# Kernel tuning notes

Hardware: AMD Instinct MI355X
Metric: run time of the kernel (lower is better)

Reference implementation:

```python
import jax, jax.numpy as jnp
import numpy as np

B, H, W, C, NH = 4, 64, 64, 512, 16
HD = C // NH
BIAS_LEVEL = 0.1
LN_EPS = 1e-5


def layernorm(x, g, b):
    m = jnp.mean(x, axis=-1, keepdims=True)
    v = jnp.mean(jnp.square(x - m), axis=-1, keepdims=True)
    return (x - m) * jax.lax.rsqrt(v + LN_EPS) * g + b


def partition(x, idx):
    # x: [B, L, C] -> windows [nW, S, C]
    xg = x.reshape(B, H, W, C)
    if idx == 0:  # horizontal strips: window = one row of length W
        return xg.reshape(B * H, W, C)
    else:  # vertical strips: window = one column of length H, ordered by column
        return xg.transpose(0, 2, 1, 3).reshape(B * W, H, C)


def unpartition(w, idx):
    # w: [nW, S, C] -> [B, L, C]
    if idx == 0:
        return w.reshape(B, H * W, C)
    else:
        return w.reshape(B, W, H, C).transpose(0, 2, 1, 3).reshape(B, H * W, C)


def eg_attention(q, k, v, res_x, rpe, idx):
    # q,k,v: [B, L, C]; res_x: [B, L, C]; rpe: [1, NH, S, S]
    S = rpe.shape[-1]
    nW = (B * H * W) // S

    def to_heads(t):
        return partition(t, idx).reshape(nW, S, NH, HD).transpose(0, 2, 1, 3)

    qh, kh, vh = to_heads(q), to_heads(k), to_heads(v)  # [nW, NH, S, HD]
    attn = jnp.einsum('whsd,whtd->whst', qh, kh) + BIAS_LEVEL * rpe
    # gating mask from raw scores
    M = jnp.mean(jnp.abs(attn), axis=(1, 2, 3), keepdims=True)  # [nW,1,1,1]
    M = M / jnp.max(M)
    M = jnp.maximum(M, 0.5)
    # L2-normalize rows, trig transform
    norm = jnp.sqrt(jnp.sum(jnp.square(attn), axis=-1, keepdims=True))
    attn = attn / jnp.maximum(norm, 1e-12)
    attn = 1.0 - jnp.cos(attn * (jnp.pi / 2))
    attn = attn * M
    out = jnp.einsum('whst,whtd->whsd', attn, vh)  # [nW, NH, S, HD]
    out = out.transpose(0, 2, 1, 3).reshape(nW, S, C)
    out = unpartition(out, idx)  # [B, L, C]
    # masked residual: res_x is chunked sequentially (row-major), as in the source
    res = res_x.reshape(nW, S, C) * (1.0 - M[:, 0])
    res = res.reshape(B, H * W, C)
    return out + res


def eg_block(x, rpe, idx, ln1_g, ln1_b, wqkv, wproj, bproj, ln2_g, ln2_b,
             wfc1, bfc1, wfc2, bfc2):
    img = layernorm(x, ln1_g, ln1_b)
    qkv = img @ wqkv  # [B, L, 3C]
    q, k, v = jnp.split(qkv, 3, axis=-1)
    att = eg_attention(q, k, v, x, rpe, idx)
    att = att @ wproj + bproj
    x = x + att
    h = layernorm(x, ln2_g, ln2_b)
    h = jax.nn.gelu(h @ wfc1 + bfc1, approximate=False) @ wfc2 + bfc2
    return x + h


def setup_inputs() -> dict:
    key = jax.random.key(0)
    ks = jax.random.split(key, 16)
    d = {
        'x': jax.random.normal(ks[0], (B, H * W, C), jnp.float32),
        'rpe0': jax.random.normal(ks[1], (1, NH, W, W), jnp.float32),
        'rpe1': jax.random.normal(ks[2], (1, NH, H, H), jnp.float32),
    }
    for i, blk in enumerate(['0', '1']):
        kk = jax.random.split(ks[3 + i], 8)
        d['ln1_g' + blk] = jnp.ones((C,), jnp.float32)
        d['ln1_b' + blk] = jnp.zeros((C,), jnp.float32)
        d['wqkv' + blk] = jax.random.normal(kk[0], (C, 3 * C), jnp.float32) * 0.02
        d['wproj' + blk] = jax.random.normal(kk[1], (C, C), jnp.float32) * 0.02
        d['bproj' + blk] = jnp.zeros((C,), jnp.float32)
        d['ln2_g' + blk] = jnp.ones((C,), jnp.float32)
        d['ln2_b' + blk] = jnp.zeros((C,), jnp.float32)
        d['wfc1_' + blk] = jax.random.normal(kk[2], (C, 4 * C), jnp.float32) * 0.02
        d['bfc1_' + blk] = jnp.zeros((4 * C,), jnp.float32)
        d['wfc2_' + blk] = jax.random.normal(kk[3], (4 * C, C), jnp.float32) * 0.02
        d['bfc2_' + blk] = jnp.zeros((C,), jnp.float32)
    return d


def reference(x, rpe0, rpe1,
              ln1_g0, ln1_b0, wqkv0, wproj0, bproj0, ln2_g0, ln2_b0,
              wfc1_0, bfc1_0, wfc2_0, bfc2_0,
              ln1_g1, ln1_b1, wqkv1, wproj1, bproj1, ln2_g1, ln2_b1,
              wfc1_1, bfc1_1, wfc2_1, bfc2_1):
    x = eg_block(x, rpe0, 0, ln1_g0, ln1_b0, wqkv0, wproj0, bproj0,
                 ln2_g0, ln2_b0, wfc1_0, bfc1_0, wfc2_0, bfc2_0)
    x = eg_block(x, rpe1, 1, ln1_g1, ln1_b1, wqkv1, wproj1, bproj1,
                 ln2_g1, ln2_b1, wfc1_1, bfc1_1, wfc2_1, bfc2_1)
    return x
```

## Files before the change

kernel.cpp:

```cpp
#include <hip/hip_runtime.h>
#include <cstdint>
#include <cstddef>

typedef __bf16 bf16;
typedef __attribute__((ext_vector_type(4))) float f32x4;
typedef __attribute__((ext_vector_type(8))) __bf16 bf16x8;
typedef __attribute__((ext_vector_type(4))) __bf16 bf16x4;

static __device__ __forceinline__ f32x4 mfma16(bf16x8 a, bf16x8 b, f32x4 c) {
    return __builtin_amdgcn_mfma_f32_16x16x32_bf16(a, b, c, 0, 0, 0);
}

#define GLOAD_LDS16(gsrc, ldst)                                              \
    __builtin_amdgcn_global_load_lds(                                        \
        (const __attribute__((address_space(1))) void*)(gsrc),               \
        (__attribute__((address_space(3))) void*)(ldst), 16, 0, 0)

struct TransArgs {
    const float* W[8];
    bf16* Wt[8];
    int K[8];
    int N[8];
    int blk0[9];
};

__global__ __launch_bounds__(256)
void transpose_all(TransArgs a) {
    __shared__ float tile[32][33];
    const int b = blockIdx.x;
    int j = 0;
    #pragma unroll
    for (int i = 0; i < 7; ++i)
        if (b >= a.blk0[i + 1]) j = i + 1;
    const int rel = b - a.blk0[j];
    const int K = a.K[j], N = a.N[j];
    const int nxb = N >> 5;
    const int n0 = (rel % nxb) * 32, k0 = (rel / nxb) * 32;
    const float* W = a.W[j];
    bf16* Wt = a.Wt[j];
    const int tx = threadIdx.x & 31, ty = threadIdx.x >> 5;
    #pragma unroll
    for (int i = ty; i < 32; i += 8)
        tile[i][tx] = W[(size_t)(k0 + i) * N + n0 + tx];
    __syncthreads();
    #pragma unroll
    for (int i = ty; i < 32; i += 8)
        Wt[(size_t)(n0 + i) * K + k0 + tx] = (bf16)tile[tx][i];
}

__global__ __launch_bounds__(256)
void ln_kernel(const float* __restrict__ x, const float* __restrict__ g,
               const float* __restrict__ b, bf16* __restrict__ out) {
    const int row = blockIdx.x * 4 + (threadIdx.x >> 6);
    const int lane = threadIdx.x & 63;
    const float* p = x + (size_t)row * 512 + lane * 8;
    const float4 a0 = *(const float4*)p;
    const float4 a1 = *(const float4*)(p + 4);
    float vx[8] = {a0.x, a0.y, a0.z, a0.w, a1.x, a1.y, a1.z, a1.w};
    float s = 0.f, ss = 0.f;
    #pragma unroll
    for (int k = 0; k < 8; ++k) { s += vx[k]; ss += vx[k] * vx[k]; }
    #pragma unroll
    for (int m = 1; m < 64; m <<= 1) {
        s  += __shfl_xor(s, m);
        ss += __shfl_xor(ss, m);
    }
    const float mean = s * (1.0f / 512.0f);
    const float var  = ss * (1.0f / 512.0f) - mean * mean;
    const float inv  = rsqrtf(var + 1e-5f);
    const int c0 = lane * 8;
    const float4 g0 = *(const float4*)&g[c0], g1 = *(const float4*)&g[c0 + 4];
    const float4 b0 = *(const float4*)&b[c0], b1 = *(const float4*)&b[c0 + 4];
    const float gv[8] = {g0.x, g0.y, g0.z, g0.w, g1.x, g1.y, g1.z, g1.w};
    const float bv[8] = {b0.x, b0.y, b0.z, b0.w, b1.x, b1.y, b1.z, b1.w};
    bf16x8 o;
    #pragma unroll
    for (int k = 0; k < 8; ++k)
        o[k] = (bf16)((vx[k] - mean) * inv * gv[k] + bv[k]);
    *(bf16x8*)&out[(size_t)row * 512 + c0] = o;
}

template <int EPI, int KT>
__global__ __launch_bounds__(512, 8)
void gemm_bt(const bf16* __restrict__ A, const bf16* __restrict__ Bt,
             int N, int Krt, const float* __restrict__ bias,
             const float* __restrict__ res, float* __restrict__ outf,
             bf16* __restrict__ outh) {
    const int K = (KT > 0) ? KT : Krt;
    __shared__ __align__(16) bf16 smem[16384];
    auto lsA = [&](int buf) { return smem + buf * 4096; };
    auto lsB = [&](int buf) { return smem + 8192 + buf * 4096; };
    const int nx = gridDim.x;
    const int nwg = nx * gridDim.y;
    const int flat = blockIdx.y * nx + blockIdx.x;
    const int cpx = nwg >> 3;
    const int bswz = (flat & 7) * cpx + (flat >> 3);
    const int bn = bswz % nx, bm = bswz / nx;

    const int tid = threadIdx.x, lane = tid & 63, wv = tid >> 6;
    const int wr = wv >> 2, wc = wv & 3;
    const int l15 = lane & 15, lg = lane >> 4;
    const size_t abase = (size_t)bm * 128 * K;
    const size_t bbase = (size_t)bn * 128 * K;
    const int sr = wv * 16 + (lane >> 2);
    const int ks = ((lane & 3) ^ ((sr >> 1) & 3)) * 8;
    const bf16* aSrc = &A[abase + (size_t)sr * K + ks];
    const bf16* bSrc = &Bt[bbase + (size_t)sr * K + ks];

    f32x4 acc[4][2] = {};

    auto stage = [&](int buf, int kt) {
        GLOAD_LDS16(aSrc + kt, lsA(buf) + wv * 512);
        GLOAD_LDS16(bSrc + kt, lsB(buf) + wv * 512);
    };
    auto compute = [&](int buf) {
        bf16x8 af[4], bfr[2];
        #pragma unroll
        for (int i = 0; i < 4; ++i) {
            const int r = wr * 64 + i * 16 + l15;
            af[i] = *(const bf16x8*)
                (lsA(buf) + r * 32 + ((lg ^ ((r >> 1) & 3)) * 8));
        }
        #pragma unroll
        for (int j = 0; j < 2; ++j) {
            const int r = wc * 32 + j * 16 + l15;
            bfr[j] = *(const bf16x8*)
                (lsB(buf) + r * 32 + ((lg ^ ((r >> 1) & 3)) * 8));
        }
        #pragma unroll
        for (int i = 0; i < 4; ++i)
            #pragma unroll
            for (int j = 0; j < 2; ++j)
                acc[i][j] = mfma16(af[i], bfr[j], acc[i][j]);
    };

    if constexpr (KT > 0) {
        constexpr int NK = KT >> 5;
        stage(0, 0);
        __syncthreads();
        #pragma unroll
        for (int t = 0; t < NK - 1; ++t) {
            stage((t + 1) & 1, (t + 1) * 32);
            compute(t & 1);
            __syncthreads();
        }
        compute((NK - 1) & 1);
        __syncthreads();
    } else {
        const int NK = K >> 5;
        stage(0, 0);
        __syncthreads();
        int cur = 0;
        for (int t = 0; t < NK - 1; ++t) {
            stage(cur ^ 1, (t + 1) * 32);
            compute(cur);
            __syncthreads();
            cur ^= 1;
        }
        compute(cur);
        __syncthreads();
    }

    float* lsW = (float*)smem + wv * 1024;
    const int orow = bm * 128 + wr * 64;
    const int ocol = bn * 128 + wc * 32;
    #pragma unroll
    for (int i = 0; i < 4; ++i) {
        #pragma unroll
        for (int r = 0; r < 4; ++r)
            #pragma unroll
            for (int j = 0; j < 2; ++j)
                lsW[(lg * 4 + r) * 36 + j * 16 + l15] = acc[i][j][r];
        __builtin_amdgcn_s_waitcnt(0);
        if constexpr (EPI == 0 || EPI == 2) {
            const int rl = lane >> 2, c8 = (lane & 3) * 8;
            const float4 v0 = *(const float4*)&lsW[rl * 36 + c8];
            const float4 v1 = *(const float4*)&lsW[rl * 36 + c8 + 4];
            float vv[8] = {v0.x, v0.y, v0.z, v0.w, v1.x, v1.y, v1.z, v1.w};
            if constexpr (EPI == 2) {
                const float4 bb0 = *(const float4*)&bias[ocol + c8];
                const float4 bb1 = *(const float4*)&bias[ocol + c8 + 4];
                const float bv[8] = {bb0.x, bb0.y, bb0.z, bb0.w,
                                     bb1.x, bb1.y, bb1.z, bb1.w};
                #pragma unroll
                for (int e = 0; e < 8; ++e) {
                    const float t = vv[e] + bv[e];
                    vv[e] = 0.5f * t * (1.0f + erff(t * 0.70710678118f));
                }
            }
            bf16x8 o;
            #pragma unroll
            for (int e = 0; e < 8; ++e) o[e] = (bf16)vv[e];
            *(bf16x8*)&outh[(size_t)(orow + i * 16 + rl) * N + ocol + c8] = o;
        } else {
            const int c4 = (lane & 7) * 4;
            const float4 bb = *(const float4*)&bias[ocol + c4];
            #pragma unroll
            for (int ii = 0; ii < 2; ++ii) {
                const int rl = ii * 8 + (lane >> 3);
                const size_t gro = (size_t)(orow + i * 16 + rl) * N + ocol + c4;
                float4 v = *(const float4*)&lsW[rl * 36 + c4];
                const float4 rr = *(const float4*)&res[gro];
                v.x += bb.x + rr.x; v.y += bb.y + rr.y;
                v.z += bb.z + rr.z; v.w += bb.w + rr.w;
                *(float4*)&outf[gro] = v;
            }
        }
    }
}

__global__ __launch_bounds__(256)
void attn_stats(const bf16* __restrict__ qkv, const float* __restrict__ rpe,
                float* __restrict__ Mraw4, int idx) {
    __shared__ float lsum[4];
    const int bid = blockIdx.x;
    const int w = bid >> 2;
    const int tid = threadIdx.x, lane = tid & 63, wv = tid >> 6;
    const int h = (bid & 3) * 4 + wv;
    const int l15 = lane & 15, lg = lane >> 4;
    const long gbase = (idx == 0) ? (long)w * 64 : ((long)(w >> 6) * 4096 + (w & 63));
    const long gstride = (idx == 0) ? 1 : 64;
    bf16x8 kf[4];
    #pragma unroll
    for (int i = 0; i < 4; ++i) {
        const long gs = gbase + (long)(i * 16 + l15) * gstride;
        kf[i] = *(const bf16x8*)&qkv[gs * 1536 + 512 + h * 32 + lg * 8];
    }
    const float* rh = rpe + h * 4096;
    float asum = 0.f;
    #pragma unroll
    for (int mi = 0; mi < 4; ++mi) {
        const long gs = gbase + (long)(mi * 16 + l15) * gstride;
        const bf16x8 qf = *(const bf16x8*)&qkv[gs * 1536 + h * 32 + lg * 8];
        f32x4 sc[4] = {};
        #pragma unroll
        for (int ni = 0; ni < 4; ++ni) sc[ni] = mfma16(qf, kf[ni], sc[ni]);
        #pragma unroll
        for (int r = 0; r < 4; ++r) {
            const int srow = mi * 16 + lg * 4 + r;
            #pragma unroll
            for (int ni = 0; ni < 4; ++ni)
                asum += fabsf(sc[ni][r] + 0.1f * rh[srow * 64 + ni * 16 + l15]);
        }
    }
    #pragma unroll
    for (int m = 1; m < 64; m <<= 1) asum += __shfl_xor(asum, m);
    if (lane == 0) lsum[wv] = asum;
    __syncthreads();
    if (tid == 0) Mraw4[bid] = lsum[0] + lsum[1] + lsum[2] + lsum[3];
}

__global__ __launch_bounds__(256)
void mcalc(const float* __restrict__ Mraw4, float* __restrict__ Mv) {
    __shared__ float red[4];
    const int t = threadIdx.x, lane = t & 63;
    const float v = (Mraw4[t * 4] + Mraw4[t * 4 + 1] + Mraw4[t * 4 + 2] +
                     Mraw4[t * 4 + 3]) * (1.0f / 65536.0f);
    float m = v;
    #pragma unroll
    for (int msk = 1; msk < 64; msk <<= 1) m = fmaxf(m, __shfl_xor(m, msk));
    if (lane == 0) red[t >> 6] = m;
    __syncthreads();
    const float mm = fmaxf(fmaxf(red[0], red[1]), fmaxf(red[2], red[3]));
    Mv[t] = fmaxf(v / mm, 0.5f);
}

__global__ __launch_bounds__(256)
void attn_apply(const bf16* __restrict__ qkv, const float* __restrict__ rpe,
                const float* __restrict__ Mv, const float* __restrict__ xin,
                bf16* __restrict__ attout, int idx) {
    __shared__ __align__(16) bf16 lsP[4][64 * 64];
    __shared__ __align__(16) bf16 lsVt[4][32 * 64];
    const int bid = blockIdx.x;
    const int w = bid >> 2;
    const int tid = threadIdx.x, lane = tid & 63, wv = tid >> 6;
    const int h = (bid & 3) * 4 + wv;
    const int l15 = lane & 15, lg = lane >> 4;
    const long gbase = (idx == 0) ? (long)w * 64 : ((long)(w >> 6) * 4096 + (w & 63));
    const long gstride = (idx == 0) ? 1 : 64;
    const float Mw = Mv[w];
    bf16* P  = lsP[wv];
    bf16* Vt = lsVt[wv];

    {
        const int d4 = (lane & 7) * 4;
        #pragma unroll
        for (int it = 0; it < 8; ++it) {
            const int t = it * 8 + (lane >> 3);
            const bf16x4 v = *(const bf16x4*)
                &qkv[(gbase + (long)t * gstride) * 1536 + 1024 + h * 32 + d4];
            #pragma unroll
            for (int e = 0; e < 4; ++e) {
                const int d = d4 + e;
                Vt[d * 64 + (t ^ ((d & 7) * 8))] = v[e];
            }
        }
    }
    bf16x8 kf[4];
    #pragma unroll
    for (int i = 0; i < 4; ++i) {
        const long gs = gbase + (long)(i * 16 + l15) * gstride;
        kf[i] = *(const bf16x8*)&qkv[gs * 1536 + 512 + h * 32 + lg * 8];
    }
    const float* rh = rpe + h * 4096;
    #pragma unroll
    for (int mi = 0; mi < 4; ++mi) {
        const long gs = gbase + (long)(mi * 16 + l15) * gstride;
        const bf16x8 qf = *(const bf16x8*)&qkv[gs * 1536 + h * 32 + lg * 8];
        f32x4 sc[4] = {};
        #pragma unroll
        for (int ni = 0; ni < 4; ++ni) sc[ni] = mfma16(qf, kf[ni], sc[ni]);
        #pragma unroll
        for (int r = 0; r < 4; ++r) {
            const int srow = mi * 16 + lg * 4 + r;
            float vv[4], ssq = 0.f;
            #pragma unroll
            for (int ni = 0; ni < 4; ++ni) {
                const float v = sc[ni][r] + 0.1f * rh[srow * 64 + ni * 16 + l15];
                vv[ni] = v;
                ssq += v * v;
            }
            ssq += __shfl_xor(ssq, 1);
            ssq += __shfl_xor(ssq, 2);
            ssq += __shfl_xor(ssq, 4);
            ssq += __shfl_xor(ssq, 8);
            const float is = 1.0f / fmaxf(sqrtf(ssq), 1e-12f);
            #pragma unroll
            for (int ni = 0; ni < 4; ++ni) {
                const float v = (1.0f - __cosf(vv[ni] * is * 1.57079632679f)) * Mw;
                const int col = ni * 16 + l15;
                P[srow * 64 + (col ^ ((srow & 7) * 8))] = (bf16)v;
            }
        }
    }
    f32x4 acc[4][2] = {};
    #pragma unroll
    for (int kk = 0; kk < 2; ++kk) {
        bf16x8 bfr[2];
        #pragma unroll
        for (int dj = 0; dj < 2; ++dj) {
            const int d = dj * 16 + l15;
            bfr[dj] = *(const bf16x8*)&Vt[d * 64 + ((kk * 32 + lg * 8) ^ ((d & 7) * 8))];
        }
        #pragma unroll
        for (int mi = 0; mi < 4; ++mi) {
            const int s = mi * 16 + l15;
            const bf16x8 af = *(const bf16x8*)&P[s * 64 + ((kk * 32 + lg * 8) ^ ((s & 7) * 8))];
            #pragma unroll
            for (int dj = 0; dj < 2; ++dj)
                acc[mi][dj] = mfma16(af, bfr[dj], acc[mi][dj]);
        }
    }
    #pragma unroll
    for (int mi = 0; mi < 4; ++mi) {
        #pragma unroll
        for (int r = 0; r < 4; ++r) {
            const int s = mi * 16 + lg * 4 + r;
            const long gg = gbase + (long)s * gstride;
            const float rm = 1.0f - Mv[(int)(gg >> 6)];
            #pragma unroll
            for (int dj = 0; dj < 2; ++dj) {
                const int d = dj * 16 + l15;
                const size_t oidx = (size_t)gg * 512 + h * 32 + d;
                attout[oidx] = (bf16)(acc[mi][dj][r] + xin[oidx] * rm);
            }
        }
    }
}

extern "C" void kernel_launch(void* const* d_in, const int* in_sizes, int n_in,
                              void* d_out, int out_size, void* d_ws, size_t ws_size,
                              hipStream_t stream) {
    const float* x    = (const float*)d_in[0];
    const float* rpe0 = (const float*)d_in[1];
    const float* rpe1 = (const float*)d_in[2];
    auto W = [&](int i) { return (const float*)d_in[i]; };

    char* ws = (char*)d_ws;
    size_t off = 0;
    auto alloc = [&](size_t bytes) {
        void* p = ws + off;
        off += (bytes + 255) & ~(size_t)255;
        return p;
    };
    bf16 *wqkvT[2], *wprojT[2], *wfc1T[2], *wfc2T[2];
    for (int b = 0; b < 2; ++b) {
        wqkvT[b] = (bf16*)alloc((size_t)1536 * 512 * 2);
        wprojT[b] = (bf16*)alloc((size_t)512 * 512 * 2);
        wfc1T[b] = (bf16*)alloc((size_t)2048 * 512 * 2);
        wfc2T[b] = (bf16*)alloc((size_t)512 * 2048 * 2);
    }
    bf16* IMG = (bf16*)alloc((size_t)16384 * 512 * 2);
    bf16* QKV = (bf16*)alloc((size_t)16384 * 1536 * 2);
    bf16* ATT = (bf16*)alloc((size_t)16384 * 512 * 2);
    bf16* H1  = QKV;
    float* X1    = (float*)alloc((size_t)16384 * 512 * 4);
    float* Mraw4 = (float*)alloc(1024 * 4);
    float* Mv    = (float*)alloc(256 * 4);
    float* XMID  = (float*)d_out;

    TransArgs ta;
    const int widx[8] = {5, 6, 10, 12, 16, 17, 21, 23};
    bf16* wdst[8] = {wqkvT[0], wprojT[0], wfc1T[0], wfc2T[0],
                     wqkvT[1], wprojT[1], wfc1T[1], wfc2T[1]};
    const int wk[8] = {512, 512, 512, 2048, 512, 512, 512, 2048};
    const int wn[8] = {1536, 512, 2048, 512, 1536, 512, 2048, 512};
    int acc_b = 0;
    for (int i = 0; i < 8; ++i) {
        ta.W[i] = W(widx[i]);
        ta.Wt[i] = wdst[i];
        ta.K[i] = wk[i];
        ta.N[i] = wn[i];
        ta.blk0[i] = acc_b;
        acc_b += (wn[i] / 32) * (wk[i] / 32);
    }
    ta.blk0[8] = acc_b;
    transpose_all<<<acc_b, 256, 0, stream>>>(ta);

    for (int b = 0; b < 2; ++b) {
        const float* xin = (b == 0) ? x : X1;
        const float* rpe = (b == 0) ? rpe0 : rpe1;
        const int base = (b == 0) ? 3 : 14;
        const float* ln1g = W(base + 0);
        const float* ln1b = W(base + 1);
        const float* bproj = W(base + 4);
        const float* ln2g = W(base + 5);
        const float* ln2b = W(base + 6);
        const float* bfc1 = W(base + 8);
        const float* bfc2 = W(base + 10);

        ln_kernel<<<4096, 256, 0, stream>>>(xin, ln1g, ln1b, IMG);
        gemm_bt<0, 512><<<dim3(12, 128), 512, 0, stream>>>(
            IMG, wqkvT[b], 1536, 512, nullptr, nullptr, nullptr, QKV);
        attn_stats<<<1024, 256, 0, stream>>>(QKV, rpe, Mraw4, b);
        mcalc<<<1, 256, 0, stream>>>(Mraw4, Mv);
        attn_apply<<<1024, 256, 0, stream>>>(QKV, rpe, Mv, xin, ATT, b);
        gemm_bt<1, 512><<<dim3(4, 128), 512, 0, stream>>>(
            ATT, wprojT[b], 512, 512, bproj, xin, XMID, nullptr);
        ln_kernel<<<4096, 256, 0, stream>>>(XMID, ln2g, ln2b, IMG);
        gemm_bt<2, 512><<<dim3(16, 128), 512, 0, stream>>>(
            IMG, wfc1T[b], 2048, 512, bfc1, nullptr, nullptr, H1);
        gemm_bt<1, 0><<<dim3(4, 128), 512, 0, stream>>>(
            H1, wfc2T[b], 512, 2048, bfc2, XMID, (b == 0) ? X1 : XMID, nullptr);
    }
    (void)in_sizes; (void)n_in; (void)out_size; (void)ws_size;
}
```

Baseline: 436.1 us.

## Store intermediate residual streams in bf16 and fold mask calc into attn_apply

New measurement: 460.2 us. 5.5% more time.

```diff
diff --git a/kernel.cpp b/kernel.cpp
--- a/kernel.cpp
+++ b/kernel.cpp
@@ -15,6 +15,20 @@
     __builtin_amdgcn_global_load_lds(                                        \
         (const __attribute__((address_space(1))) void*)(gsrc),               \
         (__attribute__((address_space(3))) void*)(ldst), 16, 0, 0)
+
+template <typename T>
+static __device__ __forceinline__ void load8(const T* p, float* v) {
+    if constexpr (sizeof(T) == 4) {
+        const float4 a0 = *(const float4*)p;
+        const float4 a1 = *(const float4*)(p + 4);
+        v[0] = a0.x; v[1] = a0.y; v[2] = a0.z; v[3] = a0.w;
+        v[4] = a1.x; v[5] = a1.y; v[6] = a1.z; v[7] = a1.w;
+    } else {
+        const bf16x8 a = *(const bf16x8*)p;
+        #pragma unroll
+        for (int e = 0; e < 8; ++e) v[e] = (float)a[e];
+    }
+}
 
 struct TransArgs {
     const float* W[8];
@@ -48,15 +62,14 @@
         Wt[(size_t)(n0 + i) * K + k0 + tx] = (bf16)tile[tx][i];
 }
 
+template <typename T>
 __global__ __launch_bounds__(256)
-void ln_kernel(const float* __restrict__ x, const float* __restrict__ g,
+void ln_kernel(const T* __restrict__ x, const float* __restrict__ g,
                const float* __restrict__ b, bf16* __restrict__ out) {
     const int row = blockIdx.x * 4 + (threadIdx.x >> 6);
     const int lane = threadIdx.x & 63;
-    const float* p = x + (size_t)row * 512 + lane * 8;
-    const float4 a0 = *(const float4*)p;
-    const float4 a1 = *(const float4*)(p + 4);
-    float vx[8] = {a0.x, a0.y, a0.z, a0.w, a1.x, a1.y, a1.z, a1.w};
+    float vx[8];
+    load8(x + (size_t)row * 512 + lane * 8, vx);
     float s = 0.f, ss = 0.f;
     #pragma unroll
     for (int k = 0; k < 8; ++k) { s += vx[k]; ss += vx[k] * vx[k]; }
@@ -80,11 +93,11 @@
     *(bf16x8*)&out[(size_t)row * 512 + c0] = o;
 }
 
-template <int EPI, int KT>
+template <int EPI, int KT, typename RT>
 __global__ __launch_bounds__(512, 8)
 void gemm_bt(const bf16* __restrict__ A, const bf16* __restrict__ Bt,
              int N, int Krt, const float* __restrict__ bias,
-             const float* __restrict__ res, float* __restrict__ outf,
+             const RT* __restrict__ res, float* __restrict__ outf,
              bf16* __restrict__ outh) {
     const int K = (KT > 0) ? KT : Krt;
     __shared__ __align__(16) bf16 smem[16384];
@@ -172,11 +185,12 @@
             for (int j = 0; j < 2; ++j)
                 lsW[(lg * 4 + r) * 36 + j * 16 + l15] = acc[i][j][r];
         __builtin_amdgcn_s_waitcnt(0);
-        if constexpr (EPI == 0 || EPI == 2) {
+        if constexpr (EPI == 0 || EPI == 2 || EPI == 3) {
             const int rl = lane >> 2, c8 = (lane & 3) * 8;
             const float4 v0 = *(const float4*)&lsW[rl * 36 + c8];
             const float4 v1 = *(const float4*)&lsW[rl * 36 + c8 + 4];
             float vv[8] = {v0.x, v0.y, v0.z, v0.w, v1.x, v1.y, v1.z, v1.w};
+            const size_t gro = (size_t)(orow + i * 16 + rl) * N + ocol + c8;
             if constexpr (EPI == 2) {
                 const float4 bb0 = *(const float4*)&bias[ocol + c8];
                 const float4 bb1 = *(const float4*)&bias[ocol + c8 + 4];
@@ -187,11 +201,20 @@
                     const float t = vv[e] + bv[e];
                     vv[e] = 0.5f * t * (1.0f + erff(t * 0.70710678118f));
                 }
+            } else if constexpr (EPI == 3) {
+                const float4 bb0 = *(const float4*)&bias[ocol + c8];
+                const float4 bb1 = *(const float4*)&bias[ocol + c8 + 4];
+                const float bv[8] = {bb0.x, bb0.y, bb0.z, bb0.w,
+                                     bb1.x, bb1.y, bb1.z, bb1.w};
+                float rv[8];
+                load8(res + gro, rv);
+                #pragma unroll
+                for (int e = 0; e < 8; ++e) vv[e] += bv[e] + rv[e];
             }
             bf16x8 o;
             #pragma unroll
             for (int e = 0; e < 8; ++e) o[e] = (bf16)vv[e];
-            *(bf16x8*)&outh[(size_t)(orow + i * 16 + rl) * N + ocol + c8] = o;
+            *(bf16x8*)&outh[gro] = o;
         } else {
             const int c4 = (lane & 7) * 4;
             const float4 bb = *(const float4*)&bias[ocol + c4];
@@ -200,9 +223,17 @@
                 const int rl = ii * 8 + (lane >> 3);
                 const size_t gro = (size_t)(orow + i * 16 + rl) * N + ocol + c4;
                 float4 v = *(const float4*)&lsW[rl * 36 + c4];
-                const float4 rr = *(const float4*)&res[gro];
-                v.x += bb.x + rr.x; v.y += bb.y + rr.y;
-                v.z += bb.z + rr.z; v.w += bb.w + rr.w;
+                float rr[4];
+                if constexpr (sizeof(RT) == 4) {
+                    const float4 r4 = *(const float4*)&res[gro];
+                    rr[0] = r4.x; rr[1] = r4.y; rr[2] = r4.z; rr[3] = r4.w;
+                } else {
+                    const bf16x4 r4 = *(const bf16x4*)&res[gro];
+                    #pragma unroll
+                    for (int e = 0; e < 4; ++e) rr[e] = (float)r4[e];
+                }
+                v.x += bb.x + rr[0]; v.y += bb.y + rr[1];
+                v.z += bb.z + rr[2]; v.w += bb.w + rr[3];
                 *(float4*)&outf[gro] = v;
             }
         }
@@ -250,27 +281,15 @@
     if (tid == 0) Mraw4[bid] = lsum[0] + lsum[1] + lsum[2] + lsum[3];
 }
 
-__global__ __launch_bounds__(256)
-void mcalc(const float* __restrict__ Mraw4, float* __restrict__ Mv) {
-    __shared__ float red[4];
-    const int t = threadIdx.x, lane = t & 63;
-    const float v = (Mraw4[t * 4] + Mraw4[t * 4 + 1] + Mraw4[t * 4 + 2] +
-                     Mraw4[t * 4 + 3]) * (1.0f / 65536.0f);
-    float m = v;
-    #pragma unroll
-    for (int msk = 1; msk < 64; msk <<= 1) m = fmaxf(m, __shfl_xor(m, msk));
-    if (lane == 0) red[t >> 6] = m;
-    __syncthreads();
-    const float mm = fmaxf(fmaxf(red[0], red[1]), fmaxf(red[2], red[3]));
-    Mv[t] = fmaxf(v / mm, 0.5f);
-}
-
+template <typename XT>
 __global__ __launch_bounds__(256)
 void attn_apply(const bf16* __restrict__ qkv, const float* __restrict__ rpe,
-                const float* __restrict__ Mv, const float* __restrict__ xin,
+                const float* __restrict__ Mraw4, const XT* __restrict__ xin,
                 bf16* __restrict__ attout, int idx) {
     __shared__ __align__(16) bf16 lsP[4][64 * 64];
     __shared__ __align__(16) bf16 lsVt[4][32 * 64];
+    __shared__ float Mvs[256];
+    __shared__ float red[4];
     const int bid = blockIdx.x;
     const int w = bid >> 2;
     const int tid = threadIdx.x, lane = tid & 63, wv = tid >> 6;
@@ -278,7 +297,21 @@
     const int l15 = lane & 15, lg = lane >> 4;
     const long gbase = (idx == 0) ? (long)w * 64 : ((long)(w >> 6) * 4096 + (w & 63));
     const long gstride = (idx == 0) ? 1 : 64;
-    const float Mw = Mv[w];
+
+    {
+        const float v = (Mraw4[tid * 4] + Mraw4[tid * 4 + 1] +
+                         Mraw4[tid * 4 + 2] + Mraw4[tid * 4 + 3]) *
+                        (1.0f / 65536.0f);
+        float m = v;
+        #pragma unroll
+        for (int msk = 1; msk < 64; msk <<= 1) m = fmaxf(m, __shfl_xor(m, msk));
+        if (lane == 0) red[wv] = m;
+        __syncthreads();
+        const float mm = fmaxf(fmaxf(red[0], red[1]), fmaxf(red[2], red[3]));
+        Mvs[tid] = fmaxf(v / mm, 0.5f);
+        __syncthreads();
+    }
+    const float Mw = Mvs[w];
     bf16* P  = lsP[wv];
     bf16* Vt = lsVt[wv];
 
@@ -357,12 +390,12 @@
         for (int r = 0; r < 4; ++r) {
             const int s = mi * 16 + lg * 4 + r;
             const long gg = gbase + (long)s * gstride;
-            const float rm = 1.0f - Mv[(int)(gg >> 6)];
+            const float rm = 1.0f - Mvs[(int)(gg >> 6)];
             #pragma unroll
             for (int dj = 0; dj < 2; ++dj) {
                 const int d = dj * 16 + l15;
                 const size_t oidx = (size_t)gg * 512 + h * 32 + d;
-                attout[oidx] = (bf16)(acc[mi][dj][r] + xin[oidx] * rm);
+                attout[oidx] = (bf16)(acc[mi][dj][r] + (float)xin[oidx] * rm);
             }
         }
     }
@@ -394,10 +427,10 @@
     bf16* QKV = (bf16*)alloc((size_t)16384 * 1536 * 2);
     bf16* ATT = (bf16*)alloc((size_t)16384 * 512 * 2);
     bf16* H1  = QKV;
-    float* X1    = (float*)alloc((size_t)16384 * 512 * 4);
+    bf16* XMID  = (bf16*)alloc((size_t)16384 * 512 * 2);
+    bf16* X1    = (bf16*)alloc((size_t)16384 * 512 * 2);
     float* Mraw4 = (float*)alloc(1024 * 4);
-    float* Mv    = (float*)alloc(256 * 4);
-    float* XMID  = (float*)d_out;
+    float* OUT   = (float*)d_out;
 
     TransArgs ta;
     const int widx[8] = {5, 6, 10, 12, 16, 17, 21, 23};
@@ -418,7 +451,6 @@
     transpose_all<<<acc_b, 256, 0, stream>>>(ta);
 
     for (int b = 0; b < 2; ++b) {
-        const float* xin = (b == 0) ? x : X1;
         const float* rpe = (b == 0) ? rpe0 : rpe1;
         const int base = (b == 0) ? 3 : 14;
         const float* ln1g = W(base + 0);
@@ -429,19 +461,35 @@
         const float* bfc1 = W(base + 8);
         const float* bfc2 = W(base + 10);
 
-        ln_kernel<<<4096, 256, 0, stream>>>(xin, ln1g, ln1b, IMG);
-        gemm_bt<0, 512><<<dim3(12, 128), 512, 0, stream>>>(
-            IMG, wqkvT[b], 1536, 512, nullptr, nullptr, nullptr, QKV);
-        attn_stats<<<1024, 256, 0, stream>>>(QKV, rpe, Mraw4, b);
-        mcalc<<<1, 256, 0, stream>>>(Mraw4, Mv);
-        attn_apply<<<1024, 256, 0, stream>>>(QKV, rpe, Mv, xin, ATT, b);
-        gemm_bt<1, 512><<<dim3(4, 128), 512, 0, stream>>>(
-            ATT, wprojT[b], 512, 512, bproj, xin, XMID, nullptr);
-        ln_kernel<<<4096, 256, 0, stream>>>(XMID, ln2g, ln2b, IMG);
-        gemm_bt<2, 512><<<dim3(16, 128), 512, 0, stream>>>(
-            IMG, wfc1T[b], 2048, 512, bfc1, nullptr, nullptr, H1);
-        gemm_bt<1, 0><<<dim3(4, 128), 512, 0, stream>>>(
-            H1, wfc2T[b], 512, 2048, bfc2, XMID, (b == 0) ? X1 : XMID, nullptr);
+        if (b == 0) {
+            ln_kernel<float><<<4096, 256, 0, stream>>>(x, ln1g, ln1b, IMG);
+            gemm_bt<0, 512, float><<<dim3(12, 128), 512, 0, stream>>>(
+                IMG, wqkvT[0], 1536, 512, nullptr, nullptr, nullptr, QKV);
+            attn_stats<<<1024, 256, 0, stream>>>(QKV, rpe, Mraw4, 0);
+            attn_apply<float><<<1024, 256, 0, stream>>>(
+                QKV, rpe, Mraw4, x, ATT, 0);
+            gemm_bt<3, 512, float><<<dim3(4, 128), 512, 0, stream>>>(
+                ATT, wprojT[0], 512, 512, bproj, x, nullptr, XMID);
+            ln_kernel<bf16><<<4096, 256, 0, stream>>>(XMID, ln2g, ln2b, IMG);
+            gemm_bt<2, 512, float><<<dim3(16, 128), 512, 0, stream>>>(
+                IMG, wfc1T[0], 2048, 512, bfc1, nullptr, nullptr, H1);
+            gemm_bt<3, 0, bf16><<<dim3(4, 128), 512, 0, stream>>>(
+                H1, wfc2T[0], 512, 2048, bfc2, XMID, nullptr, X1);
+        } else {
+            ln_kernel<bf16><<<4096, 256, 0, stream>>>(X1, ln1g, ln1b, IMG);
+            gemm_bt<0, 512, float><<<dim3(12, 128), 512, 0, stream>>>(
+                IMG, wqkvT[1], 1536, 512, nullptr, nullptr, nullptr, QKV);
+            attn_stats<<<1024, 256, 0, stream>>>(QKV, rpe, Mraw4, 1);
+            attn_apply<bf16><<<1024, 256, 0, stream>>>(
+                QKV, rpe, Mraw4, X1, ATT, 1);
+            gemm_bt<3, 512, bf16><<<dim3(4, 128), 512, 0, stream>>>(
+                ATT, wprojT[1], 512, 512, bproj, X1, nullptr, XMID);
+            ln_kernel<bf16><<<4096, 256, 0, stream>>>(XMID, ln2g, ln2b, IMG);
+            gemm_bt<2, 512, float><<<dim3(16, 128), 512, 0, stream>>>(
+                IMG, wfc1T[1], 2048, 512, bfc1, nullptr, nullptr, H1);
+            gemm_bt<1, 0, bf16><<<dim3(4, 128), 512, 0, stream>>>(
+                H1, wfc2T[1], 512, 2048, bfc2, XMID, OUT, nullptr);
+        }
     }
     (void)in_sizes; (void)n_in; (void)out_size; (void)ws_size;
 }
```
